# Kernel tuning notes

Hardware: AMD Instinct MI355X
Metric: run time of the kernel (lower is better)

Reference implementation:

```python
import jax, jax.numpy as jnp
import numpy as np

N_EMBD = 1024
N_HEAD = 16
HEAD_DIM = N_EMBD // N_HEAD
EPS = 1e-5


def setup_inputs() -> dict:
    key = jax.random.key(0)
    ks = jax.random.split(key, 12)
    B, T, E = 4, 2048, N_EMBD
    s = 0.02
    return {
        "x": jax.random.normal(ks[0], (B, T, E), jnp.float32),
        "ln1_g": jnp.ones((E,), jnp.float32),
        "ln1_b": jnp.zeros((E,), jnp.float32),
        "w_attn": jax.random.normal(ks[1], (E, 3 * E), jnp.float32) * s,
        "b_attn": jnp.zeros((3 * E,), jnp.float32),
        "w_attnproj": jax.random.normal(ks[2], (E, E), jnp.float32) * s,
        "b_attnproj": jnp.zeros((E,), jnp.float32),
        "ln2_g": jnp.ones((E,), jnp.float32),
        "ln2_b": jnp.zeros((E,), jnp.float32),
        "w_fc": jax.random.normal(ks[3], (E, 4 * E), jnp.float32) * s,
        "b_fc": jnp.zeros((4 * E,), jnp.float32),
        "w_proj": jax.random.normal(ks[4], (4 * E, E), jnp.float32) * s,
        "b_proj": jnp.zeros((E,), jnp.float32),
    }


def _layernorm(x, g, b):
    mu = jnp.mean(x, axis=-1, keepdims=True)
    var = jnp.mean(jnp.square(x - mu), axis=-1, keepdims=True)
    return (x - mu) * jax.lax.rsqrt(var + EPS) * g + b


def _attention(x, w_attn, b_attn, w_attnproj, b_attnproj):
    B, T, E = x.shape
    qkv = x @ w_attn + b_attn  # [B,T,3E]
    q, k, v = jnp.split(qkv, 3, axis=-1)
    q = q.reshape(B, T, N_HEAD, HEAD_DIM).transpose(0, 2, 1, 3)
    k = k.reshape(B, T, N_HEAD, HEAD_DIM).transpose(0, 2, 1, 3)
    v = v.reshape(B, T, N_HEAD, HEAD_DIM).transpose(0, 2, 1, 3)
    scores = jnp.einsum("bhqd,bhkd->bhqk", q, k) / np.sqrt(HEAD_DIM).astype(np.float32)
    causal = jnp.tril(jnp.ones((T, T), bool))
    scores = jnp.where(causal, scores, -jnp.inf)
    attn = jax.nn.softmax(scores, axis=-1)
    out = jnp.einsum("bhqk,bhkd->bhqd", attn, v)
    out = out.transpose(0, 2, 1, 3).reshape(B, T, E)
    return out @ w_attnproj + b_attnproj


def reference(x, ln1_g, ln1_b, w_attn, b_attn, w_attnproj, b_attnproj,
              ln2_g, ln2_b, w_fc, b_fc, w_proj, b_proj):
    x = x + _attention(_layernorm(x, ln1_g, ln1_b), w_attn, b_attn,
                       w_attnproj, b_attnproj)
    h = _layernorm(x, ln2_g, ln2_b)
    h = jax.nn.gelu(h @ w_fc + b_fc, approximate=False)
    x = x + (h @ w_proj + b_proj)
    return x
```

## Files before the change

### kernel.cpp

```cpp
#include <hip/hip_runtime.h>
#include <math.h>


constexpr int E_    = 1024;
constexpr int NHEAD = 16;
constexpr int BATCH = 4;
constexpr int TSEQ  = 2048;
constexpr int MROWS = BATCH * TSEQ;

typedef unsigned short ushort_t;
typedef short  bf16x8 __attribute__((ext_vector_type(8)));
typedef float  f32x4  __attribute__((ext_vector_type(4)));
typedef unsigned short u16x4 __attribute__((ext_vector_type(4)));
typedef unsigned short u16x8 __attribute__((ext_vector_type(8)));

__device__ __forceinline__ ushort_t f2bf(float f) {
  unsigned u = __float_as_uint(f);
  unsigned r = (u + 0x7fffu + ((u >> 16) & 1u)) >> 16;
  return (ushort_t)r;
}

__device__ __forceinline__ void gload_lds16(const void* g, void* l) {
  __builtin_amdgcn_global_load_lds(
      (const __attribute__((address_space(1))) void*)g,
      (__attribute__((address_space(3))) void*)l, 16, 0, 0);
}

__global__ __launch_bounds__(256) void castT_kernel(const float* __restrict__ W,
                                                    ushort_t* __restrict__ Wt,
                                                    int K, int N) {
  const int n = blockIdx.x * 64 + (threadIdx.x & 63);
  const int k = blockIdx.y * 32 + (threadIdx.x >> 6) * 8;
  ushort_t v[8];
  #pragma unroll
  for (int u = 0; u < 8; ++u) v[u] = f2bf(W[(size_t)(k + u) * N + n]);
  *(u16x8*)&Wt[(size_t)n * K + k] = *(const u16x8*)v;
}

__global__ __launch_bounds__(256) void ln_kernel(const float* __restrict__ x,
                                                 const float* __restrict__ g,
                                                 const float* __restrict__ b,
                                                 ushort_t* __restrict__ y) {
  const int row = blockIdx.x;
  const float4* xr = reinterpret_cast<const float4*>(x + (size_t)row * E_);
  float4 v = xr[threadIdx.x];
  float s  = v.x + v.y + v.z + v.w;
  float ss = v.x * v.x + v.y * v.y + v.z * v.z + v.w * v.w;
  #pragma unroll
  for (int off = 32; off > 0; off >>= 1) {
    s  += __shfl_down(s, off);
    ss += __shfl_down(ss, off);
  }
  __shared__ float red[8];
  __shared__ float stats[2];
  const int wid = threadIdx.x >> 6;
  if ((threadIdx.x & 63) == 0) { red[wid] = s; red[4 + wid] = ss; }
  __syncthreads();
  if (threadIdx.x == 0) {
    float S  = red[0] + red[1] + red[2] + red[3];
    float SS = red[4] + red[5] + red[6] + red[7];
    float mu  = S * (1.0f / E_);
    float var = SS * (1.0f / E_) - mu * mu;
    stats[0] = mu;
    stats[1] = rsqrtf(var + 1e-5f);
  }
  __syncthreads();
  const float mu = stats[0], rstd = stats[1];
  float4 gv = reinterpret_cast<const float4*>(g)[threadIdx.x];
  float4 bv = reinterpret_cast<const float4*>(b)[threadIdx.x];
  u16x4 o;
  o[0] = f2bf((v.x - mu) * rstd * gv.x + bv.x);
  o[1] = f2bf((v.y - mu) * rstd * gv.y + bv.y);
  o[2] = f2bf((v.z - mu) * rstd * gv.z + bv.z);
  o[3] = f2bf((v.w - mu) * rstd * gv.w + bv.w);
  *(u16x4*)(y + (size_t)row * E_ + threadIdx.x * 4) = o;
}

template <int BN, int WM, int WN, int GELU, int RES, int OBF>
__global__ __launch_bounds__(512) void gemm2_kernel(
    const ushort_t* __restrict__ A, const ushort_t* __restrict__ Wt,
    const float* __restrict__ bias, const float* __restrict__ res,
    void* __restrict__ Cout, int M, int N, int K) {
  constexpr int BM = 256, BK = 64;
  constexpr int WMR = BM / WM;
  constexpr int WNC = BN / WN;
  constexpr int MR  = WMR / 16;
  constexpr int NR  = WNC / 16;
  extern __shared__ ushort_t smem[];
  ushort_t* As = smem;
  ushort_t* Bs = smem + 2 * BM * BK;

  const int t = threadIdx.x, lane = t & 63, w = t >> 6;
  const int wr = w / WN, wc = w % WN;
  const int bm = blockIdx.y * BM, bn = blockIdx.x * BN;
  const int l15 = lane & 15, l4 = lane >> 4;

  f32x4 acc[MR][NR];
  #pragma unroll
  for (int mi = 0; mi < MR; ++mi)
    #pragma unroll
    for (int ni = 0; ni < NR; ++ni) acc[mi][ni] = f32x4{0.f, 0.f, 0.f, 0.f};

  const ushort_t* gA = A  + (size_t)(bm + (t >> 3)) * K + (t & 7) * 8;
  const ushort_t* gB = Wt + (size_t)(bn + (t >> 3)) * K + (t & 7) * 8;

  auto stage = [&](int buf, int k0) {
    #pragma unroll
    for (int i = 0; i < BM / 64; ++i)
      gload_lds16(gA + (size_t)(i * 64) * K + k0,
                  As + buf * BM * BK + (i * 64 + w * 8) * BK);
    #pragma unroll
    for (int i = 0; i < BN / 64; ++i)
      gload_lds16(gB + (size_t)(i * 64) * K + k0,
                  Bs + buf * BN * BK + (i * 64 + w * 8) * BK);
  };

  stage(0, 0);
  __syncthreads();
  int cur = 0;
  for (int k0 = 0; k0 < K; k0 += BK) {
    if (k0 + BK < K) stage(cur ^ 1, k0 + BK);
    #pragma unroll
    for (int kk = 0; kk < 2; ++kk) {
      bf16x8 af[MR], bv[NR];
      #pragma unroll
      for (int mi = 0; mi < MR; ++mi)
        af[mi] = *(const bf16x8*)&As[cur * BM * BK +
                 (wr * WMR + mi * 16 + l15) * BK + kk * 32 + l4 * 8];
      #pragma unroll
      for (int ni = 0; ni < NR; ++ni)
        bv[ni] = *(const bf16x8*)&Bs[cur * BN * BK +
                 (wc * WNC + ni * 16 + l15) * BK + kk * 32 + l4 * 8];
      #pragma unroll
      for (int mi = 0; mi < MR; ++mi)
        #pragma unroll
        for (int ni = 0; ni < NR; ++ni)
          acc[mi][ni] = __builtin_amdgcn_mfma_f32_16x16x32_bf16(
              af[mi], bv[ni], acc[mi][ni], 0, 0, 0);
    }
    __syncthreads();
    cur ^= 1;
  }

  float biasv[NR];
  #pragma unroll
  for (int ni = 0; ni < NR; ++ni)
    biasv[ni] = bias[bn + wc * WNC + ni * 16 + l15];
  const int ccol = bn + wc * WNC + l15;

  #pragma unroll
  for (int mi = 0; mi < MR; ++mi) {
    #pragma unroll
    for (int j = 0; j < 4; ++j) {
      const int row = bm + wr * WMR + mi * 16 + l4 * 4 + j;
      const size_t rbase = (size_t)row * N;
      #pragma unroll
      for (int ni = 0; ni < NR; ++ni) {
        float v = acc[mi][ni][j] + biasv[ni];
        if (GELU) v = 0.5f * v * (1.0f + erff(v * 0.70710678118654752f));
        if (RES)  v += res[rbase + ccol + ni * 16];
        if (OBF)  ((ushort_t*)Cout)[rbase + ccol + ni * 16] = f2bf(v);
        else      ((float*)Cout)[rbase + ccol + ni * 16] = v;
      }
    }
  }
}

__global__ __launch_bounds__(256) void attn_kernel(const ushort_t* __restrict__ qkv,
                                                   ushort_t* __restrict__ out) {
  __shared__ ushort_t Ks[2][64 * 64];
  __shared__ ushort_t Vt[2][64 * 64];
  __shared__ ushort_t Ps[4][32 * 64];

  constexpr float CSCL = 0.18033688011112042f;
  constexpr float THR2 = 11.5415603f;

  const int qb  = (int)gridDim.x - 1 - (int)blockIdx.x;
  const int b   = blockIdx.y >> 4;
  const int hd  = blockIdx.y & 15;
  const int t   = threadIdx.x;
  const int lane = t & 63, w = t >> 6;
  const int l15 = lane & 15, l4 = lane >> 4;

  const size_t rs3 = 3 * E_;
  const ushort_t* base = qkv + (size_t)b * TSEQ * rs3 + hd * 64;
  const int q0w = qb * 128 + w * 32;

  const int srow = t >> 2;
  const int sc0  = (t & 3) << 4;

  bf16x8 qf[2][2];
  #pragma unroll
  for (int qs = 0; qs < 2; ++qs)
    #pragma unroll
    for (int kk = 0; kk < 2; ++kk)
      qf[qs][kk] = *(const bf16x8*)(base +
          (size_t)(q0w + qs * 16 + l15) * rs3 + kk * 32 + l4 * 8);

  float mrun[2], lrun[2];
  f32x4 oacc[2][4];
  #pragma unroll
  for (int qs = 0; qs < 2; ++qs) {
    mrun[qs] = -INFINITY; lrun[qs] = 0.f;
    #pragma unroll
    for (int c = 0; c < 4; ++c) oacc[qs][c] = f32x4{0.f, 0.f, 0.f, 0.f};
  }

  u16x8 v0, v1;

  auto loadV = [&](int kt) {
    const ushort_t* vsrc = base + 2 * E_ + (size_t)(kt * 64 + srow) * rs3 + sc0;
    v0 = *(const u16x8*)vsrc;
    v1 = *(const u16x8*)(vsrc + 8);
  };
  auto stageK = [&](int kt, int buf) {
    #pragma unroll
    for (int c = 0; c < 2; ++c) {
      const int lrow  = w * 16 + c * 8 + (lane >> 3);
      const int chunk = (lane & 7) ^ (lane >> 3);
      gload_lds16(base + E_ + (size_t)(kt * 64 + lrow) * rs3 + chunk * 8,
                  &Ks[buf][(w * 16 + c * 8) * 64]);
    }
  };
  auto writeVt = [&](int buf) {
    #pragma unroll
    for (int j = 0; j < 8; ++j) {
      const int d0 = sc0 + j;
      const int d1 = sc0 + 8 + j;
      Vt[buf][d0 * 64 + (srow ^ (((d0 + (d0 >> 4)) & 7) << 3))] = v0[j];
      Vt[buf][d1 * 64 + (srow ^ (((d1 + (d1 >> 4)) & 7) << 3))] = v1[j];
    }
  };

  loadV(0);
  stageK(0, 0);
  writeVt(0);
  __syncthreads();

  const int nt = 2 * qb + 2;
  int cur = 0;
  const f32x4 zero = {0.f, 0.f, 0.f, 0.f};

  for (int kt = 0; kt < nt; ++kt) {
    if (kt + 1 < nt) { loadV(kt + 1); stageK(kt + 1, cur ^ 1); }

    const int ktb = kt * 64;
    if (ktb <= q0w + 31) {
      f32x4 s[2][4];
      #pragma unroll
      for (int ct = 0; ct < 4; ++ct) {
        const int krow = ct * 16 + l15;
        const int ksw  = (krow & 7) << 3;
        bf16x8 kf0 = *(const bf16x8*)&Ks[cur][krow * 64 + ((l4 * 8) ^ ksw)];
        bf16x8 kf1 = *(const bf16x8*)&Ks[cur][krow * 64 + ((32 + l4 * 8) ^ ksw)];
        #pragma unroll
        for (int qs = 0; qs < 2; ++qs) {
          f32x4 a0 = __builtin_amdgcn_mfma_f32_16x16x32_bf16(kf0, qf[qs][0], zero, 0, 0, 0);
          s[qs][ct] = __builtin_amdgcn_mfma_f32_16x16x32_bf16(kf1, qf[qs][1], a0, 0, 0, 0);
        }
      }

      const bool domask = (ktb + 63 > q0w);
      #pragma unroll
      for (int qs = 0; qs < 2; ++qs)
        #pragma unroll
        for (int ct = 0; ct < 4; ++ct) {
          s[qs][ct] *= CSCL;
          if (domask) {
            const int q = q0w + qs * 16 + l15;
            #pragma unroll
            for (int r = 0; r < 4; ++r)
              if (ktb + ct * 16 + l4 * 4 + r > q) s[qs][ct][r] = -INFINITY;
          }
        }

      #pragma unroll
      for (int qs = 0; qs < 2; ++qs) {
        float pmax = s[qs][0][0];
        #pragma unroll
        for (int ct = 0; ct < 4; ++ct)
          #pragma unroll
          for (int r = 0; r < 4; ++r) pmax = fmaxf(pmax, s[qs][ct][r]);
        pmax = fmaxf(pmax, __shfl_xor(pmax, 16));
        pmax = fmaxf(pmax, __shfl_xor(pmax, 32));
        if (!__all(pmax - mrun[qs] <= THR2)) {
          const float mnew = fmaxf(mrun[qs], pmax);
          const float esc  = exp2f(mrun[qs] - mnew);
          mrun[qs] = mnew;
          lrun[qs] *= esc;
          #pragma unroll
          for (int r = 0; r < 4; ++r) {
            const float eo = __shfl(esc, l4 * 4 + r);
            #pragma unroll
            for (int c = 0; c < 4; ++c) oacc[qs][c][r] *= eo;
          }
        }
        float rs = 0.f;
        #pragma unroll
        for (int ct = 0; ct < 4; ++ct)
          #pragma unroll
          for (int r = 0; r < 4; ++r) {
            const float pv = exp2f(s[qs][ct][r] - mrun[qs]);
            s[qs][ct][r] = pv;
            rs += pv;
          }
        rs += __shfl_xor(rs, 16);
        rs += __shfl_xor(rs, 32);
        lrun[qs] += rs;
      }

      const int psw = (l15 & 7) << 3;
      #pragma unroll
      for (int qs = 0; qs < 2; ++qs)
        #pragma unroll
        for (int ct = 0; ct < 4; ++ct) {
          u16x4 pk;
          #pragma unroll
          for (int r = 0; r < 4; ++r) pk[r] = f2bf(s[qs][ct][r]);
          *(u16x4*)&Ps[w][(qs * 16 + l15) * 64 + ((ct * 16 + l4 * 4) ^ psw)] = pk;
        }

      bf16x8 pa[2][2];
      #pragma unroll
      for (int qs = 0; qs < 2; ++qs)
        #pragma unroll
        for (int kk = 0; kk < 2; ++kk)
          pa[qs][kk] = *(const bf16x8*)&Ps[w][(qs * 16 + l15) * 64 +
                                              ((kk * 32 + l4 * 8) ^ psw)];

      #pragma unroll
      for (int ct2 = 0; ct2 < 4; ++ct2) {
        const int d   = ct2 * 16 + l15;
        const int vsw = ((d + (d >> 4)) & 7) << 3;
        bf16x8 vb0 = *(const bf16x8*)&Vt[cur][d * 64 + ((l4 * 8) ^ vsw)];
        bf16x8 vb1 = *(const bf16x8*)&Vt[cur][d * 64 + ((32 + l4 * 8) ^ vsw)];
        #pragma unroll
        for (int qs = 0; qs < 2; ++qs) {
          oacc[qs][ct2] = __builtin_amdgcn_mfma_f32_16x16x32_bf16(
              pa[qs][0], vb0, oacc[qs][ct2], 0, 0, 0);
          oacc[qs][ct2] = __builtin_amdgcn_mfma_f32_16x16x32_bf16(
              pa[qs][1], vb1, oacc[qs][ct2], 0, 0, 0);
        }
      }
    }

    if (kt + 1 < nt) writeVt(cur ^ 1);
    __syncthreads();
    cur ^= 1;
  }

  #pragma unroll
  for (int qs = 0; qs < 2; ++qs)
    #pragma unroll
    for (int r = 0; r < 4; ++r) {
      const float lr  = __shfl(lrun[qs], l4 * 4 + r);
      const float inv = 1.0f / lr;
      const int qg = q0w + qs * 16 + l4 * 4 + r;
      ushort_t* dst = out + (size_t)(b * TSEQ + qg) * E_ + hd * 64 + l15;
      #pragma unroll
      for (int ct2 = 0; ct2 < 4; ++ct2)
        dst[ct2 * 16] = f2bf(oacc[qs][ct2][r] * inv);
    }
}

extern "C" void kernel_launch(void* const* d_in, const int* in_sizes, int n_in,
                              void* d_out, int out_size, void* d_ws, size_t ws_size,
                              hipStream_t stream) {
  const float* x          = (const float*)d_in[0];
  const float* ln1_g      = (const float*)d_in[1];
  const float* ln1_b      = (const float*)d_in[2];
  const float* w_attn     = (const float*)d_in[3];
  const float* b_attn     = (const float*)d_in[4];
  const float* w_attnproj = (const float*)d_in[5];
  const float* b_attnproj = (const float*)d_in[6];
  const float* ln2_g      = (const float*)d_in[7];
  const float* ln2_b      = (const float*)d_in[8];
  const float* w_fc       = (const float*)d_in[9];
  const float* b_fc       = (const float*)d_in[10];
  const float* w_proj     = (const float*)d_in[11];
  const float* b_proj     = (const float*)d_in[12];
  float* out = (float*)d_out;

  char* ws = (char*)d_ws;
  const size_t MB = 1024 * 1024;
  ushort_t* qkv      = (ushort_t*)ws;
  ushort_t* h_bf     = (ushort_t*)ws;
  ushort_t* xn       = (ushort_t*)(ws + 64 * MB);
  ushort_t* attnout  = (ushort_t*)(ws + 80 * MB);
  float*    x1       = (float*)(ws + 96 * MB);
  ushort_t* w_attnT  = (ushort_t*)(ws + 128 * MB);
  ushort_t* w_aprojT = w_attnT  + (size_t)3 * E_ * E_;
  ushort_t* w_fcT    = w_aprojT + (size_t)E_ * E_;
  ushort_t* w_projT  = w_fcT    + (size_t)4 * E_ * E_;

  constexpr int SM256 = (256 + 256) * 64 * 2 * 2;
  constexpr int SM128 = (256 + 128) * 64 * 2 * 2;
  hipFuncSetAttribute((const void*)gemm2_kernel<256, 2, 4, 0, 0, 1>,
                      hipFuncAttributeMaxDynamicSharedMemorySize, SM256);
  hipFuncSetAttribute((const void*)gemm2_kernel<256, 2, 4, 1, 0, 1>,
                      hipFuncAttributeMaxDynamicSharedMemorySize, SM256);
  hipFuncSetAttribute((const void*)gemm2_kernel<128, 4, 2, 0, 1, 0>,
                      hipFuncAttributeMaxDynamicSharedMemorySize, SM128);

  castT_kernel<<<dim3(3 * E_ / 64, E_ / 32), 256, 0, stream>>>(w_attn, w_attnT, E_, 3 * E_);
  castT_kernel<<<dim3(E_ / 64, E_ / 32), 256, 0, stream>>>(w_attnproj, w_aprojT, E_, E_);
  castT_kernel<<<dim3(4 * E_ / 64, E_ / 32), 256, 0, stream>>>(w_fc, w_fcT, E_, 4 * E_);
  castT_kernel<<<dim3(E_ / 64, 4 * E_ / 32), 256, 0, stream>>>(w_proj, w_projT, 4 * E_, E_);

  ln_kernel<<<MROWS, 256, 0, stream>>>(x, ln1_g, ln1_b, xn);
  gemm2_kernel<256, 2, 4, 0, 0, 1><<<dim3(3 * E_ / 256, MROWS / 256), 512, SM256, stream>>>(
      xn, w_attnT, b_attn, nullptr, qkv, MROWS, 3 * E_, E_);
  attn_kernel<<<dim3(TSEQ / 128, BATCH * NHEAD), 256, 0, stream>>>(qkv, attnout);
  gemm2_kernel<128, 4, 2, 0, 1, 0><<<dim3(E_ / 128, MROWS / 256), 512, SM128, stream>>>(
      attnout, w_aprojT, b_attnproj, x, x1, MROWS, E_, E_);
  ln_kernel<<<MROWS, 256, 0, stream>>>(x1, ln2_g, ln2_b, xn);
  gemm2_kernel<256, 2, 4, 1, 0, 1><<<dim3(4 * E_ / 256, MROWS / 256), 512, SM256, stream>>>(
      xn, w_fcT, b_fc, nullptr, h_bf, MROWS, 4 * E_, E_);
  gemm2_kernel<128, 4, 2, 0, 1, 0><<<dim3(E_ / 128, MROWS / 256), 512, SM128, stream>>>(
      h_bf, w_projT, b_proj, x1, out, MROWS, E_, 4 * E_);
}
```

Before: 641.7 us.

## Swizzle GEMM LDS layout, remap workgroups across XCDs, single-buffer attention V

In the GEMM, global-to-LDS copies now write XOR-swizzled columns and the fragment reads apply the same swizzle, which is meant to cut LDS bank conflicts. Both kernels also remap the linear workgroup id so that consecutive tiles are spread across the 8 XCDs, aiming for better L2 locality. The attention kernel shrinks the transposed-V buffer to a single buffer, which lowers LDS use and may raise occupancy. In exchange it adds an extra __syncthreads per key tile. The attention remap hardcodes 16 query blocks, and the swizzle assumes the workgroup count is divisible by 8.

```diff
diff --git a/kernel.cpp b/kernel.cpp
--- a/kernel.cpp
+++ b/kernel.cpp
@@ -92,8 +92,15 @@
 
   const int t = threadIdx.x, lane = t & 63, w = t >> 6;
   const int wr = w / WN, wc = w % WN;
-  const int bm = blockIdx.y * BM, bn = blockIdx.x * BN;
+
+  const int nwg = gridDim.x * gridDim.y;
+  const int lin = blockIdx.y * gridDim.x + blockIdx.x;
+  const int swz = (lin & 7) * (nwg >> 3) + (lin >> 3);
+  const int bm  = (swz / gridDim.x) * BM;
+  const int bn  = (swz % gridDim.x) * BN;
+
   const int l15 = lane & 15, l4 = lane >> 4;
+  const int sw16 = (l15 & 7) << 3;
 
   f32x4 acc[MR][NR];
   #pragma unroll
@@ -101,8 +108,9 @@
     #pragma unroll
     for (int ni = 0; ni < NR; ++ni) acc[mi][ni] = f32x4{0.f, 0.f, 0.f, 0.f};
 
-  const ushort_t* gA = A  + (size_t)(bm + (t >> 3)) * K + (t & 7) * 8;
-  const ushort_t* gB = Wt + (size_t)(bn + (t >> 3)) * K + (t & 7) * 8;
+  const int scol = ((t & 7) ^ ((t >> 3) & 7)) * 8;
+  const ushort_t* gA = A  + (size_t)(bm + (t >> 3)) * K + scol;
+  const ushort_t* gB = Wt + (size_t)(bn + (t >> 3)) * K + scol;
 
   auto stage = [&](int buf, int k0) {
     #pragma unroll
@@ -126,11 +134,11 @@
       #pragma unroll
       for (int mi = 0; mi < MR; ++mi)
         af[mi] = *(const bf16x8*)&As[cur * BM * BK +
-                 (wr * WMR + mi * 16 + l15) * BK + kk * 32 + l4 * 8];
+                 (wr * WMR + mi * 16 + l15) * BK + ((kk * 32 + l4 * 8) ^ sw16)];
       #pragma unroll
       for (int ni = 0; ni < NR; ++ni)
         bv[ni] = *(const bf16x8*)&Bs[cur * BN * BK +
-                 (wc * WNC + ni * 16 + l15) * BK + kk * 32 + l4 * 8];
+                 (wc * WNC + ni * 16 + l15) * BK + ((kk * 32 + l4 * 8) ^ sw16)];
       #pragma unroll
       for (int mi = 0; mi < MR; ++mi)
         #pragma unroll
@@ -169,15 +177,20 @@
 __global__ __launch_bounds__(256) void attn_kernel(const ushort_t* __restrict__ qkv,
                                                    ushort_t* __restrict__ out) {
   __shared__ ushort_t Ks[2][64 * 64];
-  __shared__ ushort_t Vt[2][64 * 64];
+  __shared__ ushort_t Vt[64 * 64];
   __shared__ ushort_t Ps[4][32 * 64];
 
   constexpr float CSCL = 0.18033688011112042f;
   constexpr float THR2 = 11.5415603f;
 
-  const int qb  = (int)gridDim.x - 1 - (int)blockIdx.x;
-  const int b   = blockIdx.y >> 4;
-  const int hd  = blockIdx.y & 15;
+  const int nwg = gridDim.x * gridDim.y;
+  const int lin = blockIdx.y * gridDim.x + blockIdx.x;
+  const int swzb = (lin & 7) * (nwg >> 3) + (lin >> 3);
+  const int bx = swzb & 15, by = swzb >> 4;
+
+  const int qb  = 15 - bx;
+  const int b   = by >> 4;
+  const int hd  = by & 15;
   const int t   = threadIdx.x;
   const int lane = t & 63, w = t >> 6;
   const int l15 = lane & 15, l4 = lane >> 4;
@@ -222,19 +235,19 @@
                   &Ks[buf][(w * 16 + c * 8) * 64]);
     }
   };
-  auto writeVt = [&](int buf) {
+  auto writeVt = [&]() {
     #pragma unroll
     for (int j = 0; j < 8; ++j) {
       const int d0 = sc0 + j;
       const int d1 = sc0 + 8 + j;
-      Vt[buf][d0 * 64 + (srow ^ (((d0 + (d0 >> 4)) & 7) << 3))] = v0[j];
-      Vt[buf][d1 * 64 + (srow ^ (((d1 + (d1 >> 4)) & 7) << 3))] = v1[j];
+      Vt[d0 * 64 + (srow ^ (((d0 + (d0 >> 4)) & 7) << 3))] = v0[j];
+      Vt[d1 * 64 + (srow ^ (((d1 + (d1 >> 4)) & 7) << 3))] = v1[j];
     }
   };
 
+  stageK(0, 0);
   loadV(0);
-  stageK(0, 0);
-  writeVt(0);
+  writeVt();
   __syncthreads();
 
   const int nt = 2 * qb + 2;
@@ -242,7 +255,7 @@
   const f32x4 zero = {0.f, 0.f, 0.f, 0.f};
 
   for (int kt = 0; kt < nt; ++kt) {
-    if (kt + 1 < nt) { loadV(kt + 1); stageK(kt + 1, cur ^ 1); }
+    if (kt + 1 < nt) { stageK(kt + 1, cur ^ 1); loadV(kt + 1); }
 
     const int ktb = kt * 64;
     if (ktb <= q0w + 31) {
@@ -332,8 +345,8 @@
       for (int ct2 = 0; ct2 < 4; ++ct2) {
         const int d   = ct2 * 16 + l15;
         const int vsw = ((d + (d >> 4)) & 7) << 3;
-        bf16x8 vb0 = *(const bf16x8*)&Vt[cur][d * 64 + ((l4 * 8) ^ vsw)];
-        bf16x8 vb1 = *(const bf16x8*)&Vt[cur][d * 64 + ((32 + l4 * 8) ^ vsw)];
+        bf16x8 vb0 = *(const bf16x8*)&Vt[d * 64 + ((l4 * 8) ^ vsw)];
+        bf16x8 vb1 = *(const bf16x8*)&Vt[d * 64 + ((32 + l4 * 8) ^ vsw)];
         #pragma unroll
         for (int qs = 0; qs < 2; ++qs) {
           oacc[qs][ct2] = __builtin_amdgcn_mfma_f32_16x16x32_bf16(
@@ -344,7 +357,8 @@
       }
     }
 
-    if (kt + 1 < nt) writeVt(cur ^ 1);
+    __syncthreads();
+    if (kt + 1 < nt) writeVt();
     __syncthreads();
     cur ^= 1;
   }
```

Result: faster. 586.7 us (-8.6%).
